# Kernel tuning notes

Hardware: AMD Instinct MI355X
Metric: run time of the kernel (lower is better)

## Reference

```python
import jax, jax.numpy as jnp
import numpy as np

GAMMA = 0.9
NUM_HEADS = 8
SCALE_BASE = 512.0
GN_EPS = 1e-5


def xpos(x):
    # Canonical RetNet XPOS rotary embedding (offset=0, downscale=False).
    B, S, D = x.shape
    half = D // 2
    scale_vec = (jnp.arange(0, D, 2, dtype=jnp.float32) + 0.4 * D) / (1.4 * D)  # [half]
    power = jnp.arange(S, dtype=jnp.float32) / SCALE_BASE                        # [S]
    scale = scale_vec[None, :] ** power[:, None]                                 # [S, half]
    inv_freq = 1.0 / (10000.0 ** (jnp.arange(half, dtype=jnp.float32) / half))
    sinusoid = jnp.arange(S, dtype=jnp.float32)[:, None] * inv_freq[None, :]     # [S, half]
    sin_s = jnp.repeat(jnp.sin(sinusoid) * scale, 2, axis=-1)                    # [S, D]
    cos_s = jnp.repeat(jnp.cos(sinusoid) * scale, 2, axis=-1)
    x1, x2 = x[..., ::2], x[..., 1::2]
    rot = jnp.stack([-x2, x1], axis=-1).reshape(x.shape)  # rotate_every_two
    return x * cos_s[None] + rot * sin_s[None]


def group_norm(x, weight, bias, num_groups):
    # x: [N, C], GroupNorm over groups of channels per sample.
    N, C = x.shape
    xg = x.reshape(N, num_groups, C // num_groups)
    mu = jnp.mean(xg, axis=-1, keepdims=True)
    var = jnp.var(xg, axis=-1, keepdims=True)
    xn = ((xg - mu) * jax.lax.rsqrt(var + GN_EPS)).reshape(N, C)
    return xn * weight[None, :] + bias[None, :]


def decay_matrix(S):
    n = jnp.arange(S, dtype=jnp.float32)[:, None]
    m = jnp.arange(S, dtype=jnp.float32)[None, :]
    return jnp.where(n >= m, GAMMA ** (n - m), 0.0)  # [S, S]


def setup_inputs() -> dict:
    key = jax.random.key(0)
    ks = jax.random.split(key, 6)
    B, S, Din, Dm = 2, 2048, 512, 512
    s = 1.0 / np.sqrt(Din)
    return {
        "X": jax.random.normal(ks[0], (B, S, Din), dtype=jnp.float32),
        "Wq": jax.random.uniform(ks[1], (Din, Dm), jnp.float32, -s, s),
        "Wk": jax.random.uniform(ks[2], (Din, Dm), jnp.float32, -s, s),
        "Wv": jax.random.uniform(ks[3], (Din, Dm), jnp.float32, -s, s),
        "gn_weight": jnp.ones((Dm,), jnp.float32),
        "gn_bias": jnp.zeros((Dm,), jnp.float32),
    }


def reference(X, Wq, Wk, Wv, gn_weight, gn_bias):
    B, S, Din = X.shape
    Dm = Wq.shape[1]
    H = NUM_HEADS
    hd = Dm // H

    q = xpos(X @ Wq)                       # [B, S, Dm]
    k = xpos(X @ Wk)
    k = group_norm(k.reshape(-1, Dm), gn_weight, gn_bias, H).reshape(B, S, Dm)
    v = X @ Wv

    # [B, H, S, hd]
    q = q.reshape(B, S, H, hd).transpose(0, 2, 1, 3)
    k = k.reshape(B, S, H, hd).transpose(0, 2, 1, 3)
    v = v.reshape(B, S, H, hd).transpose(0, 2, 1, 3)

    q = q * jax.nn.sigmoid(q)              # swish-gated queries
    scores = jnp.einsum("bhsd,bhtd->bhst", q, k)  # no scale (use_scale=False)
    msr = scores * decay_matrix(S)[None, None]    # causal decay mask
    out = jnp.einsum("bhst,bhtd->bhsd", msr, v)

    out = out.transpose(0, 2, 1, 3).reshape(B, S, Dm)
    out = out + X                           # residual (input_dim == MSR_dim -> identity)
    return jax.nn.relu(out)
```

## Files before the change

### kernel.cpp

```cpp
#include <hip/hip_runtime.h>
#include <hip/hip_bf16.h>
#include <math.h>

#define NB 2
#define SEQ 2048
#define DMODEL 512
#define NH 8
#define HDIM 64
#define NROWS (NB*SEQ)
#define HALF 256
#define NT 3

typedef __attribute__((ext_vector_type(8))) short short8;
typedef __attribute__((ext_vector_type(4))) float f32x4;
typedef __attribute__((ext_vector_type(8))) unsigned short ushort8_t;

__device__ __forceinline__ unsigned short f2bf(float f) {
  union { float f; unsigned u; } v; v.f = f;
  unsigned r = v.u + 0x7fffu + ((v.u >> 16) & 1u);
  return (unsigned short)(r >> 16);
}
__device__ __forceinline__ float bf2f(unsigned short h) {
  union { unsigned u; float f; } v; v.u = ((unsigned)h) << 16;
  return v.f;
}

__device__ __forceinline__ void gload16(const void* g, void* l) {
  __builtin_amdgcn_global_load_lds(
      (const __attribute__((address_space(1))) unsigned int*)g,
      (__attribute__((address_space(3))) unsigned int*)l, 16, 0, 0);
}

__global__ __launch_bounds__(256) void k_prep(
    const float* __restrict__ X, const float* __restrict__ Wq,
    const float* __restrict__ Wk, const float* __restrict__ Wv,
    float2* __restrict__ tab, unsigned short* __restrict__ Xb,
    unsigned short* __restrict__ Wtq, unsigned short* __restrict__ Wtk,
    unsigned short* __restrict__ Wtv) {
  __shared__ float lds[64][65];
  int blk = blockIdx.x, t = threadIdx.x;
  if (blk < 512) {
    int base = (blk * 256 + t) * 4;
    int s = base >> 8, i0 = base & 255;
    float ps = (float)s * (1.0f / 512.0f);
    float fs = (float)s;
    float2 o[4];
    for (int u = 0; u < 4; ++u) {
      int i = i0 + u;
      float sv = (2.0f * (float)i + 204.8f) * (1.0f / 716.8f);
      float scale = exp2f(ps * __log2f(sv));
      float inv_freq = exp2f((float)i * (-13.287712379549449f / 256.0f));
      float theta = fs * inv_freq;
      o[u] = make_float2(__sinf(theta) * scale, __cosf(theta) * scale);
    }
    *(float4*)&tab[base]     = make_float4(o[0].x, o[0].y, o[1].x, o[1].y);
    *(float4*)&tab[base + 2] = make_float4(o[2].x, o[2].y, o[3].x, o[3].y);
  } else if (blk < 2560) {
    int base = ((blk - 512) * 256 + t) * 4;
    float4 v = *(const float4*)(X + base);
    ushort4 o;
    o.x = f2bf(v.x); o.y = f2bf(v.y); o.z = f2bf(v.z); o.w = f2bf(v.w);
    *(ushort4*)(Xb + base) = o;
  } else {
    int wb = blk - 2560;
    int which = wb >> 6;
    const float* W = which == 0 ? Wq : which == 1 ? Wk : Wv;
    unsigned short* Wt = which == 0 ? Wtq : which == 1 ? Wtk : Wtv;
    int tile = wb & 63;
    int tk = tile & 7, tn = tile >> 3;
    int k0 = tk * 64, n0 = tn * 64;
    for (int j = 0; j < 16; ++j) {
      int e = t + 256 * j;
      int r = e >> 6, c = e & 63;
      lds[r][c] = W[(size_t)(k0 + r) * DMODEL + (n0 + c)];
    }
    __syncthreads();
    for (int j = 0; j < 16; ++j) {
      int e = t + 256 * j;
      int r = e >> 6, c = e & 63;
      Wt[(size_t)(n0 + r) * DMODEL + (k0 + c)] = f2bf(lds[c][r]);
    }
  }
}

#define BM 128
#define BN 128
#define BK 64
__global__ __launch_bounds__(256) void k_gemm(
    const unsigned short* __restrict__ A,
    const unsigned short* __restrict__ Btq, const unsigned short* __restrict__ Btk,
    const unsigned short* __restrict__ Btv,
    unsigned short* __restrict__ outq, unsigned short* __restrict__ outk,
    unsigned short* __restrict__ outvt) {
  int z = blockIdx.z;
  const unsigned short* Bt = (z == 0) ? Btq : (z == 1) ? Btk : Btv;
  __shared__ unsigned short Alds[BM * BK];
  __shared__ unsigned short Blds[BN * BK];
  int m0 = blockIdx.y * BM, n0 = blockIdx.x * BN;
  int t = threadIdx.x, lane = t & 63, w = t >> 6;
  int wr = w >> 1, wc = w & 1;
  f32x4 acc[4][4] = {};
  for (int k0 = 0; k0 < DMODEL; k0 += BK) {
    __syncthreads();
    for (int j = 0; j < 4; ++j) {
      int chunk = w * 256 + j * 64 + lane;
      int r = chunk >> 3, cl = chunk & 7, cg = cl ^ (r & 7);
      gload16(&A[(size_t)(m0 + r) * DMODEL + k0 + cg * 8],
              &Alds[(w * 256 + j * 64) * 8]);
      gload16(&Bt[(size_t)(n0 + r) * DMODEL + k0 + cg * 8],
              &Blds[(w * 256 + j * 64) * 8]);
    }
    __syncthreads();
    for (int kk = 0; kk < 2; ++kk) {
      int ch = kk * 4 + (lane >> 4);
      short8 af[4], bfr[4];
      for (int mf = 0; mf < 4; ++mf) {
        int row = wr * 64 + mf * 16 + (lane & 15);
        af[mf] = *(const short8*)&Alds[row * 64 + ((ch ^ (row & 7)) * 8)];
      }
      for (int nf = 0; nf < 4; ++nf) {
        int row = wc * 64 + nf * 16 + (lane & 15);
        bfr[nf] = *(const short8*)&Blds[row * 64 + ((ch ^ (row & 7)) * 8)];
      }
      for (int mf = 0; mf < 4; ++mf)
        for (int nf = 0; nf < 4; ++nf)
          acc[mf][nf] = __builtin_amdgcn_mfma_f32_16x16x32_bf16(af[mf], bfr[nf], acc[mf][nf], 0, 0, 0);
    }
  }
  if (z < 2) {
    unsigned short* out = (z == 0) ? outq : outk;
    for (int mf = 0; mf < 4; ++mf)
      for (int nf = 0; nf < 4; ++nf)
        for (int j = 0; j < 4; ++j) {
          int m = m0 + wr * 64 + mf * 16 + (lane >> 4) * 4 + j;
          int n = n0 + wc * 64 + nf * 16 + (lane & 15);
          out[(size_t)m * DMODEL + n] = f2bf(acc[mf][nf][j]);
        }
  } else {
    for (int mf = 0; mf < 4; ++mf)
      for (int nf = 0; nf < 4; ++nf) {
        int m = m0 + wr * 64 + mf * 16 + (lane >> 4) * 4;
        int n = n0 + wc * 64 + nf * 16 + (lane & 15);
        int b = m >> 11, s = m & (SEQ - 1);
        int h = n >> 6, d = n & 63;
        ushort4 pk;
        pk.x = f2bf(acc[mf][nf][0]); pk.y = f2bf(acc[mf][nf][1]);
        pk.z = f2bf(acc[mf][nf][2]); pk.w = f2bf(acc[mf][nf][3]);
        *(ushort4*)&outvt[((size_t)((b * NH + h) * HDIM + d)) * SEQ + s] = pk;
      }
  }
}

__global__ __launch_bounds__(256) void k_qk_transform(
    unsigned short* __restrict__ qb, unsigned short* __restrict__ kb,
    const float2* __restrict__ tab,
    const float* __restrict__ gnw, const float* __restrict__ gnb) {
  int lane = threadIdx.x & 63;
  int w = threadIdx.x >> 6;
  int row = blockIdx.x * 4 + w;
  int isk = blockIdx.y;
  unsigned short* buf = isk ? kb : qb;
  int s = row & (SEQ - 1);
  size_t off = (size_t)row * DMODEL + lane * 8;
  ushort8_t raw = *(const ushort8_t*)&buf[off];
  float v[8], r[8];
  for (int j = 0; j < 8; ++j) v[j] = bf2f(raw[j]);
  float4 t0 = *(const float4*)&tab[s * HALF + lane * 4];
  float4 t1 = *(const float4*)&tab[s * HALF + lane * 4 + 2];
  float sn[4] = {t0.x, t0.z, t1.x, t1.z};
  float cs[4] = {t0.y, t0.w, t1.y, t1.w};
  for (int p = 0; p < 4; ++p) {
    float x1 = v[2 * p], x2 = v[2 * p + 1];
    r[2 * p]     = x1 * cs[p] - x2 * sn[p];
    r[2 * p + 1] = x2 * cs[p] + x1 * sn[p];
  }
  if (!isk) {
    for (int j = 0; j < 8; ++j) r[j] = r[j] / (1.0f + __expf(-r[j]));
  } else {
    float sum = 0.0f, sq = 0.0f;
    for (int j = 0; j < 8; ++j) { sum += r[j]; sq += r[j] * r[j]; }
    for (int m = 1; m < 8; m <<= 1) { sum += __shfl_xor(sum, m); sq += __shfl_xor(sq, m); }
    float mu = sum * (1.0f / 64.0f);
    float var = sq * (1.0f / 64.0f) - mu * mu;
    float rstd = rsqrtf(var + 1e-5f);
    float4 w0 = *(const float4*)&gnw[lane * 8];
    float4 w1 = *(const float4*)&gnw[lane * 8 + 4];
    float4 b0 = *(const float4*)&gnb[lane * 8];
    float4 b1 = *(const float4*)&gnb[lane * 8 + 4];
    float wv[8] = {w0.x, w0.y, w0.z, w0.w, w1.x, w1.y, w1.z, w1.w};
    float bv[8] = {b0.x, b0.y, b0.z, b0.w, b1.x, b1.y, b1.z, b1.w};
    for (int j = 0; j < 8; ++j) r[j] = (r[j] - mu) * rstd * wv[j] + bv[j];
  }
  ushort8_t o;
  for (int j = 0; j < 8; ++j) o[j] = f2bf(r[j]);
  *(ushort8_t*)&buf[off] = o;
}

__global__ __launch_bounds__(256) void k_attn(
    const unsigned short* __restrict__ q, const unsigned short* __restrict__ k,
    const unsigned short* __restrict__ vt, const float* __restrict__ X,
    float* __restrict__ out) {
  __shared__ unsigned short klds[NT][64 * 64];
  __shared__ unsigned short vlds[NT][64 * 64];
  __shared__ unsigned short plds[4][16][72];
  int qt = blockIdx.x;
  int bh = blockIdx.y;
  int b = bh >> 3, h = bh & 7;
  int t = threadIdx.x, lane = t & 63, w = t >> 6;
  int n0 = qt * 64;
  int nw = n0 + w * 16;
  int g = lane >> 4;
  const float log2g = -0.15200309344504997f;
  short8 aq[2];
  for (int kk = 0; kk < 2; ++kk) {
    size_t off = ((size_t)(b * SEQ + nw + (lane & 15))) * DMODEL + h * HDIM + kk * 32 + g * 8;
    aq[kk] = *(const short8*)&q[off];
  }
  int kt_lo = qt - (NT - 1); if (kt_lo < 0) kt_lo = 0;
  int ntiles = qt - kt_lo + 1;
  for (int tt = 0; tt < ntiles; ++tt) {
    int m0 = (kt_lo + tt) * 64;
    for (int j = 0; j < 2; ++j) {
      int chunk = w * 128 + j * 64 + lane;
      int r = chunk >> 3, cl = chunk & 7, cg = cl ^ (r & 7);
      gload16(&k[((size_t)(b * SEQ + m0 + r)) * DMODEL + h * HDIM + cg * 8],
              &klds[tt][(w * 128 + j * 64) * 8]);
      gload16(&vt[((size_t)((b * NH + h) * HDIM + r)) * SEQ + m0 + cg * 8],
              &vlds[tt][(w * 128 + j * 64) * 8]);
    }
  }
  float sk[4];
  for (int nf = 0; nf < 4; ++nf)
    sk[nf] = exp2f(-(float)(nf * 16 + (lane & 15)) * log2g);
  int nrb = nw + g * 4;
  f32x4 o[4] = {};
  __syncthreads();
  for (int tt = 0; tt < ntiles; ++tt) {
    int m0 = (kt_lo + tt) * 64;
    float sq_[4];
    for (int j = 0; j < 4; ++j)
      sq_[j] = exp2f((float)(nrb + j - m0) * log2g);
    f32x4 sc[4] = {};
    for (int kk = 0; kk < 2; ++kk) {
      int ch = kk * 4 + g;
      for (int nf = 0; nf < 4; ++nf) {
        int row = nf * 16 + (lane & 15);
        short8 bk = *(const short8*)&klds[tt][row * 64 + ((ch ^ (row & 7)) * 8)];
        sc[nf] = __builtin_amdgcn_mfma_f32_16x16x32_bf16(aq[kk], bk, sc[nf], 0, 0, 0);
      }
    }
    for (int nf = 0; nf < 4; ++nf) {
      int cin = nf * 16 + (lane & 15);
      for (int j = 0; j < 4; ++j) {
        int dlt = nrb + j - (m0 + cin);
        float f = (dlt >= 0) ? sq_[j] * sk[nf] : 0.0f;
        plds[w][g * 4 + j][cin] = f2bf(sc[nf][j] * f);
      }
    }
    for (int kk = 0; kk < 2; ++kk) {
      int ch = kk * 4 + g;
      short8 pa = *(const short8*)&plds[w][lane & 15][kk * 32 + g * 8];
      for (int nf = 0; nf < 4; ++nf) {
        int row = nf * 16 + (lane & 15);
        short8 bv = *(const short8*)&vlds[tt][row * 64 + ((ch ^ (row & 7)) * 8)];
        o[nf] = __builtin_amdgcn_mfma_f32_16x16x32_bf16(pa, bv, o[nf], 0, 0, 0);
      }
    }
  }
  for (int nf = 0; nf < 4; ++nf)
    for (int j = 0; j < 4; ++j) {
      int srow = nw + g * 4 + j;
      int col = h * HDIM + nf * 16 + (lane & 15);
      size_t off = ((size_t)(b * SEQ + srow)) * DMODEL + col;
      float val = o[nf][j] + X[off];
      out[off] = val > 0.0f ? val : 0.0f;
    }
}

extern "C" void kernel_launch(void* const* d_in, const int* in_sizes, int n_in,
                              void* d_out, int out_size, void* d_ws, size_t ws_size,
                              hipStream_t stream) {
  const float* X   = (const float*)d_in[0];
  const float* Wq  = (const float*)d_in[1];
  const float* Wk  = (const float*)d_in[2];
  const float* Wv  = (const float*)d_in[3];
  const float* gnw = (const float*)d_in[4];
  const float* gnb = (const float*)d_in[5];
  float* out = (float*)d_out;
  char* ws = (char*)d_ws;

  float2*         tab  = (float2*)ws;
  unsigned short* Xb   = (unsigned short*)(ws + (4u << 20));
  unsigned short* Wtq  = (unsigned short*)(ws + (8u << 20));
  unsigned short* Wtk  = Wtq + 512 * 512;
  unsigned short* Wtv  = Wtk + 512 * 512;
  unsigned short* qb   = (unsigned short*)(ws + (8u << 20) + 3u * 512 * 512 * 2);
  unsigned short* kb   = qb + (size_t)NROWS * DMODEL;
  unsigned short* vt   = kb + (size_t)NROWS * DMODEL;

  k_prep<<<dim3(2752), dim3(256), 0, stream>>>(X, Wq, Wk, Wv, tab, Xb, Wtq, Wtk, Wtv);
  k_gemm<<<dim3(4, 32, 3), dim3(256), 0, stream>>>(Xb, Wtq, Wtk, Wtv, qb, kb, vt);
  k_qk_transform<<<dim3(1024, 2), dim3(256), 0, stream>>>(qb, kb, tab, gnw, gnb);
  k_attn<<<dim3(32, 16), dim3(256), 0, stream>>>(qb, kb, vt, X, out);
}
```

Measured before the change: 40.62 us.

## Fuse xpos/swish/groupnorm into attention kernel and double-buffer GEMM LDS

```diff
diff --git a/kernel.cpp b/kernel.cpp
--- a/kernel.cpp
+++ b/kernel.cpp
@@ -86,6 +86,7 @@
 #define BM 128
 #define BN 128
 #define BK 64
+#define KSTEPS (DMODEL / BK)
 __global__ __launch_bounds__(256) void k_gemm(
     const unsigned short* __restrict__ A,
     const unsigned short* __restrict__ Btq, const unsigned short* __restrict__ Btk,
@@ -94,38 +95,50 @@
     unsigned short* __restrict__ outvt) {
   int z = blockIdx.z;
   const unsigned short* Bt = (z == 0) ? Btq : (z == 1) ? Btk : Btv;
-  __shared__ unsigned short Alds[BM * BK];
-  __shared__ unsigned short Blds[BN * BK];
+  __shared__ unsigned short Alds[2][BM * BK];
+  __shared__ unsigned short Blds[2][BN * BK];
   int m0 = blockIdx.y * BM, n0 = blockIdx.x * BN;
   int t = threadIdx.x, lane = t & 63, w = t >> 6;
   int wr = w >> 1, wc = w & 1;
   f32x4 acc[4][4] = {};
-  for (int k0 = 0; k0 < DMODEL; k0 += BK) {
-    __syncthreads();
-    for (int j = 0; j < 4; ++j) {
-      int chunk = w * 256 + j * 64 + lane;
-      int r = chunk >> 3, cl = chunk & 7, cg = cl ^ (r & 7);
-      gload16(&A[(size_t)(m0 + r) * DMODEL + k0 + cg * 8],
-              &Alds[(w * 256 + j * 64) * 8]);
-      gload16(&Bt[(size_t)(n0 + r) * DMODEL + k0 + cg * 8],
-              &Blds[(w * 256 + j * 64) * 8]);
-    }
-    __syncthreads();
+
+  for (int j = 0; j < 4; ++j) {
+    int chunk = w * 256 + j * 64 + lane;
+    int r = chunk >> 3, cl = chunk & 7, cg = cl ^ (r & 7);
+    gload16(&A[(size_t)(m0 + r) * DMODEL + cg * 8], &Alds[0][(w * 256 + j * 64) * 8]);
+    gload16(&Bt[(size_t)(n0 + r) * DMODEL + cg * 8], &Blds[0][(w * 256 + j * 64) * 8]);
+  }
+  __syncthreads();
+  int cur = 0;
+  for (int ks = 0; ks < KSTEPS; ++ks) {
+    if (ks + 1 < KSTEPS) {
+      int k0 = (ks + 1) * BK;
+      for (int j = 0; j < 4; ++j) {
+        int chunk = w * 256 + j * 64 + lane;
+        int r = chunk >> 3, cl = chunk & 7, cg = cl ^ (r & 7);
+        gload16(&A[(size_t)(m0 + r) * DMODEL + k0 + cg * 8],
+                &Alds[cur ^ 1][(w * 256 + j * 64) * 8]);
+        gload16(&Bt[(size_t)(n0 + r) * DMODEL + k0 + cg * 8],
+                &Blds[cur ^ 1][(w * 256 + j * 64) * 8]);
+      }
+    }
     for (int kk = 0; kk < 2; ++kk) {
       int ch = kk * 4 + (lane >> 4);
       short8 af[4], bfr[4];
       for (int mf = 0; mf < 4; ++mf) {
         int row = wr * 64 + mf * 16 + (lane & 15);
-        af[mf] = *(const short8*)&Alds[row * 64 + ((ch ^ (row & 7)) * 8)];
+        af[mf] = *(const short8*)&Alds[cur][row * 64 + ((ch ^ (row & 7)) * 8)];
       }
       for (int nf = 0; nf < 4; ++nf) {
         int row = wc * 64 + nf * 16 + (lane & 15);
-        bfr[nf] = *(const short8*)&Blds[row * 64 + ((ch ^ (row & 7)) * 8)];
+        bfr[nf] = *(const short8*)&Blds[cur][row * 64 + ((ch ^ (row & 7)) * 8)];
       }
       for (int mf = 0; mf < 4; ++mf)
         for (int nf = 0; nf < 4; ++nf)
           acc[mf][nf] = __builtin_amdgcn_mfma_f32_16x16x32_bf16(af[mf], bfr[nf], acc[mf][nf], 0, 0, 0);
     }
+    __syncthreads();
+    cur ^= 1;
   }
   if (z < 2) {
     unsigned short* out = (z == 0) ? outq : outk;
@@ -151,55 +164,13 @@
   }
 }
 
-__global__ __launch_bounds__(256) void k_qk_transform(
-    unsigned short* __restrict__ qb, unsigned short* __restrict__ kb,
-    const float2* __restrict__ tab,
-    const float* __restrict__ gnw, const float* __restrict__ gnb) {
-  int lane = threadIdx.x & 63;
-  int w = threadIdx.x >> 6;
-  int row = blockIdx.x * 4 + w;
-  int isk = blockIdx.y;
-  unsigned short* buf = isk ? kb : qb;
-  int s = row & (SEQ - 1);
-  size_t off = (size_t)row * DMODEL + lane * 8;
-  ushort8_t raw = *(const ushort8_t*)&buf[off];
-  float v[8], r[8];
-  for (int j = 0; j < 8; ++j) v[j] = bf2f(raw[j]);
-  float4 t0 = *(const float4*)&tab[s * HALF + lane * 4];
-  float4 t1 = *(const float4*)&tab[s * HALF + lane * 4 + 2];
-  float sn[4] = {t0.x, t0.z, t1.x, t1.z};
-  float cs[4] = {t0.y, t0.w, t1.y, t1.w};
-  for (int p = 0; p < 4; ++p) {
-    float x1 = v[2 * p], x2 = v[2 * p + 1];
-    r[2 * p]     = x1 * cs[p] - x2 * sn[p];
-    r[2 * p + 1] = x2 * cs[p] + x1 * sn[p];
-  }
-  if (!isk) {
-    for (int j = 0; j < 8; ++j) r[j] = r[j] / (1.0f + __expf(-r[j]));
-  } else {
-    float sum = 0.0f, sq = 0.0f;
-    for (int j = 0; j < 8; ++j) { sum += r[j]; sq += r[j] * r[j]; }
-    for (int m = 1; m < 8; m <<= 1) { sum += __shfl_xor(sum, m); sq += __shfl_xor(sq, m); }
-    float mu = sum * (1.0f / 64.0f);
-    float var = sq * (1.0f / 64.0f) - mu * mu;
-    float rstd = rsqrtf(var + 1e-5f);
-    float4 w0 = *(const float4*)&gnw[lane * 8];
-    float4 w1 = *(const float4*)&gnw[lane * 8 + 4];
-    float4 b0 = *(const float4*)&gnb[lane * 8];
-    float4 b1 = *(const float4*)&gnb[lane * 8 + 4];
-    float wv[8] = {w0.x, w0.y, w0.z, w0.w, w1.x, w1.y, w1.z, w1.w};
-    float bv[8] = {b0.x, b0.y, b0.z, b0.w, b1.x, b1.y, b1.z, b1.w};
-    for (int j = 0; j < 8; ++j) r[j] = (r[j] - mu) * rstd * wv[j] + bv[j];
-  }
-  ushort8_t o;
-  for (int j = 0; j < 8; ++j) o[j] = f2bf(r[j]);
-  *(ushort8_t*)&buf[off] = o;
-}
-
 __global__ __launch_bounds__(256) void k_attn(
     const unsigned short* __restrict__ q, const unsigned short* __restrict__ k,
     const unsigned short* __restrict__ vt, const float* __restrict__ X,
+    const float2* __restrict__ tab,
+    const float* __restrict__ gnw, const float* __restrict__ gnb,
     float* __restrict__ out) {
+  __shared__ unsigned short qlds[64 * 64];
   __shared__ unsigned short klds[NT][64 * 64];
   __shared__ unsigned short vlds[NT][64 * 64];
   __shared__ unsigned short plds[4][16][72];
@@ -211,13 +182,15 @@
   int nw = n0 + w * 16;
   int g = lane >> 4;
   const float log2g = -0.15200309344504997f;
-  short8 aq[2];
-  for (int kk = 0; kk < 2; ++kk) {
-    size_t off = ((size_t)(b * SEQ + nw + (lane & 15))) * DMODEL + h * HDIM + kk * 32 + g * 8;
-    aq[kk] = *(const short8*)&q[off];
-  }
   int kt_lo = qt - (NT - 1); if (kt_lo < 0) kt_lo = 0;
   int ntiles = qt - kt_lo + 1;
+
+  for (int j = 0; j < 2; ++j) {
+    int chunk = w * 128 + j * 64 + lane;
+    int r = chunk >> 3, cl = chunk & 7, cg = cl ^ (r & 7);
+    gload16(&q[((size_t)(b * SEQ + n0 + r)) * DMODEL + h * HDIM + cg * 8],
+            &qlds[(w * 128 + j * 64) * 8]);
+  }
   for (int tt = 0; tt < ntiles; ++tt) {
     int m0 = (kt_lo + tt) * 64;
     for (int j = 0; j < 2; ++j) {
@@ -229,12 +202,77 @@
               &vlds[tt][(w * 128 + j * 64) * 8]);
     }
   }
+  __syncthreads();
+
+  int nrows = 64 + ntiles * 64;
+  if (t < nrows) {
+    bool isq = (t < 64);
+    int kr = t - 64;
+    int tt = kr >> 6, rr = isq ? t : (kr & 63);
+    unsigned short* base = isq ? qlds : &klds[tt][0];
+    int s_abs = isq ? (n0 + rr) : ((kt_lo + tt) * 64 + rr);
+    float x[64];
+    #pragma unroll
+    for (int c = 0; c < 8; ++c) {
+      ushort8_t u = *(const ushort8_t*)&base[(rr * 8 + (c ^ (rr & 7))) * 8];
+      #pragma unroll
+      for (int e = 0; e < 8; ++e) x[c * 8 + e] = bf2f(u[e]);
+    }
+    const float4* tb = (const float4*)&tab[(size_t)s_abs * HALF + h * 32];
+    #pragma unroll
+    for (int p2 = 0; p2 < 16; ++p2) {
+      float4 tc = tb[p2];
+      float x1 = x[4 * p2], x2 = x[4 * p2 + 1];
+      x[4 * p2]     = x1 * tc.y - x2 * tc.x;
+      x[4 * p2 + 1] = x2 * tc.y + x1 * tc.x;
+      x1 = x[4 * p2 + 2]; x2 = x[4 * p2 + 3];
+      x[4 * p2 + 2] = x1 * tc.w - x2 * tc.z;
+      x[4 * p2 + 3] = x2 * tc.w + x1 * tc.z;
+    }
+    if (isq) {
+      #pragma unroll
+      for (int c = 0; c < 64; ++c) x[c] = x[c] / (1.0f + __expf(-x[c]));
+    } else {
+      float s1 = 0.0f, s2 = 0.0f;
+      #pragma unroll
+      for (int c = 0; c < 64; ++c) { s1 += x[c]; s2 += x[c] * x[c]; }
+      float mu = s1 * (1.0f / 64.0f);
+      float var = s2 * (1.0f / 64.0f) - mu * mu;
+      float rstd = rsqrtf(var + 1e-5f);
+      const float4* gw = (const float4*)&gnw[h * HDIM];
+      const float4* gb = (const float4*)&gnb[h * HDIM];
+      #pragma unroll
+      for (int c4 = 0; c4 < 16; ++c4) {
+        float4 wv = gw[c4], bv = gb[c4];
+        x[c4 * 4 + 0] = (x[c4 * 4 + 0] - mu) * rstd * wv.x + bv.x;
+        x[c4 * 4 + 1] = (x[c4 * 4 + 1] - mu) * rstd * wv.y + bv.y;
+        x[c4 * 4 + 2] = (x[c4 * 4 + 2] - mu) * rstd * wv.z + bv.z;
+        x[c4 * 4 + 3] = (x[c4 * 4 + 3] - mu) * rstd * wv.w + bv.w;
+      }
+    }
+    #pragma unroll
+    for (int c = 0; c < 8; ++c) {
+      ushort8_t o;
+      #pragma unroll
+      for (int e = 0; e < 8; ++e) o[e] = f2bf(x[c * 8 + e]);
+      *(ushort8_t*)&base[(rr * 8 + (c ^ (rr & 7))) * 8] = o;
+    }
+  }
+  __syncthreads();
+
+  short8 aq[2];
+  {
+    int qrow = w * 16 + (lane & 15);
+    for (int kk = 0; kk < 2; ++kk) {
+      int slot = (kk * 4 + g) ^ (qrow & 7);
+      aq[kk] = *(const short8*)&qlds[(qrow * 8 + slot) * 8];
+    }
+  }
   float sk[4];
   for (int nf = 0; nf < 4; ++nf)
     sk[nf] = exp2f(-(float)(nf * 16 + (lane & 15)) * log2g);
   int nrb = nw + g * 4;
   f32x4 o[4] = {};
-  __syncthreads();
   for (int tt = 0; tt < ntiles; ++tt) {
     int m0 = (kt_lo + tt) * 64;
     float sq_[4];
@@ -300,6 +338,5 @@
 
   k_prep<<<dim3(2752), dim3(256), 0, stream>>>(X, Wq, Wk, Wv, tab, Xb, Wtq, Wtk, Wtv);
   k_gemm<<<dim3(4, 32, 3), dim3(256), 0, stream>>>(Xb, Wtq, Wtk, Wtv, qb, kb, vt);
-  k_qk_transform<<<dim3(1024, 2), dim3(256), 0, stream>>>(qb, kb, tab, gnw, gnb);
-  k_attn<<<dim3(32, 16), dim3(256), 0, stream>>>(qb, kb, vt, X, out);
-}
+  k_attn<<<dim3(32, 16), dim3(256), 0, stream>>>(qb, kb, vt, X, tab, gnw, gnb, out);
+}
```

Result: slower. 47.77 us (+17.6%).
